# Kernel optimization log

Hardware: AMD Instinct MI355X
Metric: run time of the kernel (lower is better)

The kernel has to match this reference:

```python
import jax, jax.numpy as jnp
import numpy as np

D = 128
H = 4
DK = D // H


def _spmm(row, col, val, x, n):
    # sparse.mm(adj, x) with adj in COO form: out[row] += val * x[col]
    return jax.ops.segment_sum(val[:, None] * x[col], row, num_segments=n)


def _arrg(h, a1_w, a1_b, a2_w, a2_b):
    return jax.nn.leaky_relu(h @ a1_w + a1_b, negative_slope=0.01) @ a2_w + a2_b


def _cross_attn(x, q_x, q_w, k_w, v_w):
    n, d = x.shape
    m = q_x.shape[0]
    q = (q_x @ q_w).reshape(m, H, DK).transpose(1, 0, 2)   # [H, Q, dk]
    k = (x @ k_w).reshape(n, H, DK).transpose(1, 0, 2)     # [H, N, dk]
    v = (q_x @ v_w).reshape(m, H, DK).transpose(1, 0, 2)   # [H, Q, dk]
    s = jnp.einsum('hnd,hqd->hnq', k, q) / jnp.sqrt(jnp.float32(DK))
    w = jax.nn.softmax(s, axis=-1)                          # softmax over queries
    out = jnp.einsum('hnq,hqd->hnd', w, v).transpose(1, 0, 2).reshape(n, d)
    return out + x


def setup_inputs() -> dict:
    key = jax.random.key(0)
    ks = iter(jax.random.split(key, 64))
    nrm = lambda shape, s=0.05: jax.random.normal(next(ks), shape, jnp.float32) * s
    inp = {}
    inp['trans_w'] = nrm((1, D)); inp['trans_b'] = nrm((D,))
    inp['g_w'] = nrm((D, D));     inp['g_b'] = nrm((D,))
    inp['qg_w'] = nrm((D, D));    inp['qg_b'] = nrm((D,))
    inp['q_w'] = nrm((D, D)); inp['k_w'] = nrm((D, D)); inp['v_w'] = nrm((D, D))
    inp['a1_w'] = nrm((D, 2 * D)); inp['a1_b'] = nrm((2 * D,))
    inp['a2_w'] = nrm((2 * D, D)); inp['a2_b'] = nrm((D,))
    inp['x0'] = jax.random.normal(next(ks), (25000,), jnp.float32)
    inp['q0'] = jax.random.normal(next(ks), (100,), jnp.float32)
    for i in (1, 2, 3):
        inp[f'xin{i}'] = jax.random.normal(next(ks), (25000,), jnp.float32)
        inp[f'qin{i}'] = jax.random.normal(next(ks), (100,), jnp.float32)
    n_sizes = {1: 50000, 2: 75000, 3: 100000}
    q_sizes = {1: 200, 2: 300, 3: 400}
    for i in (1, 2, 3):
        e = 16 * n_sizes[i]
        inp[f'aval{i}'] = jax.random.uniform(next(ks), (e,), jnp.float32)
        inp[f'arow{i}'] = jax.random.randint(next(ks), (e,), 0, n_sizes[i], jnp.int64)
        inp[f'acol{i}'] = jax.random.randint(next(ks), (e,), 0, n_sizes[i], jnp.int64)
        qe = 16 * q_sizes[i]
        inp[f'qval{i}'] = jax.random.uniform(next(ks), (qe,), jnp.float32)
        inp[f'qrow{i}'] = jax.random.randint(next(ks), (qe,), 0, q_sizes[i], jnp.int64)
        inp[f'qcol{i}'] = jax.random.randint(next(ks), (qe,), 0, q_sizes[i], jnp.int64)
    return inp


def reference(trans_w, trans_b, g_w, g_b, qg_w, qg_b, q_w, k_w, v_w,
              a1_w, a1_b, a2_w, a2_b,
              x0, q0, xin1, xin2, xin3, qin1, qin2, qin3,
              aval1, aval2, aval3, qval1, qval2, qval3,
              arow1, acol1, arow2, acol2, arow3, acol3,
              qrow1, qcol1, qrow2, qcol2, qrow3, qcol3):
    trans = lambda v: v[:, None] @ trans_w + trans_b
    x = trans(x0)
    qx = trans(q0)
    steps = [
        (xin1, qin1, arow1, acol1, aval1, qrow1, qcol1, qval1, 50000, 200),
        (xin2, qin2, arow2, acol2, aval2, qrow2, qcol2, qval2, 75000, 300),
        (xin3, qin3, arow3, acol3, aval3, qrow3, qcol3, qval3, 100000, 400),
    ]
    for xin, qin, ar, ac, av, qr, qc, qv, n, m in steps:
        x = jnp.concatenate([x, trans(xin)], axis=0)
        qx = jnp.concatenate([qx, trans(qin)], axis=0)
        x = _spmm(ar, ac, av, x @ g_w + g_b, n)
        qx = _spmm(qr, qc, qv, qx @ qg_w + qg_b, m)
        x = _arrg(x, a1_w, a1_b, a2_w, a2_b)
        qx = _arrg(qx, a1_w, a1_b, a2_w, a2_b)
        x = _cross_attn(x, qx, q_w, k_w, v_w)
    return (x, qx)
```

## Files before the change

### kernel.cpp

```cpp
#include <hip/hip_runtime.h>

typedef unsigned short u16;
typedef __attribute__((ext_vector_type(8))) short bf16x8;
typedef __attribute__((ext_vector_type(4))) float f32x4;
typedef __attribute__((ext_vector_type(2))) unsigned u32x2;

__device__ __forceinline__ float b2f(u16 v) {
    return __uint_as_float(((unsigned)v) << 16);
}
__device__ __forceinline__ u16 f2b(float x) {
    unsigned u = __float_as_uint(x);
    unsigned r = u + 0x7FFFu + ((u >> 16) & 1u);
    return (u16)(r >> 16);
}
__device__ __forceinline__ float4 load_bf4(const u16* p) {
    ushort4 q = *(const ushort4*)p;
    float4 f;
    f.x = b2f(q.x); f.y = b2f(q.y); f.z = b2f(q.z); f.w = b2f(q.w);
    return f;
}
__device__ __forceinline__ float4 in4(const void* p, long off, bool bf) {
    if (bf) return load_bf4((const u16*)p + off);
    return *(const float4*)((const float*)p + off);
}
__device__ __forceinline__ float in1(const void* p, long off, bool bf) {
    if (bf) return b2f(((const u16*)p)[off]);
    return ((const float*)p)[off];
}
__device__ __forceinline__ int inIdx(const void* p, long i, bool i64) {
    return ((const int*)p)[i64 ? 2 * i : i];
}

__global__ void sniff_kernel(const u16* __restrict__ x0bits, const int* __restrict__ arow,
                             int* __restrict__ flags) {
    if (threadIdx.x != 0 || blockIdx.x != 0) return;
    int plaus = 0;
    for (int i = 0; i < 256; ++i) {
        u16 v = x0bits[i];
        int e = (v >> 7) & 0xFF;
        if (v == 0 || (e >= 100 && e <= 135)) plaus++;
    }
    flags[0] = (plaus >= 200) ? 1 : 0;
    int nz = 0;
    for (int i = 1; i < 128; i += 2) nz += (arow[i] != 0);
    flags[1] = (nz == 0) ? 1 : 0;
}

__global__ void trans_kernel(const void* __restrict__ v, const void* __restrict__ tw,
                             const void* __restrict__ tb, float* __restrict__ out,
                             int rows, const int* __restrict__ flags) {
    const bool bf = flags[0] != 0;
    int t = blockIdx.x * blockDim.x + threadIdx.x;
    int c4 = (t & 31) * 4;
    int r = t >> 5;
    if (r >= rows) return;
    float vv = in1(v, r, bf);
    float4 w4 = in4(tw, c4, bf);
    float4 b4 = in4(tb, c4, bf);
    float4 o;
    o.x = vv * w4.x + b4.x; o.y = vv * w4.y + b4.y;
    o.z = vv * w4.z + b4.z; o.w = vv * w4.w + b4.w;
    *(float4*)(out + (size_t)r * 128 + c4) = o;
}

__global__ void wprep_kernel(const void* __restrict__ src, u16* __restrict__ dst,
                             int K, int N, const int* __restrict__ flags) {
    const bool bf = flags[0] != 0;
    int idx = blockIdx.x * blockDim.x + threadIdx.x;
    if (idx >= K * N) return;
    int j = idx & 7, lane = (idx >> 3) & 63, t = idx >> 9;
    int KC = K >> 5;
    int kc = t % KC, ct = t / KC;
    int k = kc * 32 + (lane >> 4) * 8 + j;
    int nn = ct * 16 + (lane & 15);
    dst[idx] = f2b(in1(src, (long)k * N + nn, bf));
}

template<int KTOT, int NOUT, bool LEAKY, typename AT, typename CT>
__launch_bounds__(256)
__global__ void gemm_mfma_kernel(const AT* __restrict__ A, const u16* __restrict__ Wf,
                                 const void* __restrict__ bias, CT* __restrict__ C,
                                 int n, const int* __restrict__ flags) {
    constexpr int KC = KTOT / 32;
    constexpr int NT = NOUT / 16;
    __shared__ u16 wlds[KTOT * NOUT];
    {
        const int4* srcw = (const int4*)Wf;
        int4* dstw = (int4*)wlds;
        constexpr int NV = KTOT * NOUT * 2 / 16;
#pragma unroll
        for (int i = 0; i < NV / 256; ++i)
            dstw[i * 256 + threadIdx.x] = srcw[i * 256 + threadIdx.x];
    }
    __syncthreads();
    const bool bf = flags[0] != 0;
    const int lane = threadIdx.x & 63;
    const int wave = threadIdx.x >> 6;
    const int quad = lane >> 4, col = lane & 15;
    const int rbase = (blockIdx.x * 4 + wave) * 16;
    if (rbase >= n) return;
    int node = rbase + col; if (node >= n) node = n - 1;
    f32x4 acc[NT];
#pragma unroll
    for (int ct = 0; ct < NT; ++ct) acc[ct] = (f32x4){0.f, 0.f, 0.f, 0.f};
#pragma unroll
    for (int kc = 0; kc < KC; ++kc) {
        bf16x8 af;
        if constexpr (sizeof(AT) == 2) {
            af = *(const bf16x8*)((const u16*)A + (size_t)node * KTOT + kc * 32 + quad * 8);
        } else {
            const float* ap = (const float*)A + (size_t)node * KTOT + kc * 32 + quad * 8;
            float4 a0 = *(const float4*)ap;
            float4 a1 = *(const float4*)(ap + 4);
            af[0] = (short)f2b(a0.x); af[1] = (short)f2b(a0.y);
            af[2] = (short)f2b(a0.z); af[3] = (short)f2b(a0.w);
            af[4] = (short)f2b(a1.x); af[5] = (short)f2b(a1.y);
            af[6] = (short)f2b(a1.z); af[7] = (short)f2b(a1.w);
        }
#pragma unroll
        for (int ct = 0; ct < NT; ++ct) {
            bf16x8 wf = *(const bf16x8*)(wlds + (((ct * KC + kc) * 64 + lane) * 8));
            acc[ct] = __builtin_amdgcn_mfma_f32_16x16x32_bf16(af, wf, acc[ct], 0, 0, 0);
        }
    }
#pragma unroll
    for (int ct = 0; ct < NT; ++ct) {
        int colg = ct * 16 + col;
        float b = bias ? in1(bias, colg, bf) : 0.f;
#pragma unroll
        for (int r = 0; r < 4; ++r) {
            int row = rbase + quad * 4 + r;
            if (row >= n) continue;
            float v = acc[ct][r] + b;
            if (LEAKY) v = v > 0.f ? v : 0.01f * v;
            if constexpr (sizeof(CT) == 2) C[(size_t)row * NOUT + colg] = (CT)f2b(v);
            else                           C[(size_t)row * NOUT + colg] = (CT)v;
        }
    }
}

__launch_bounds__(256)
__global__ void gemm_qv_kernel(const float* __restrict__ A, const u16* __restrict__ Wfq,
                               const u16* __restrict__ Wfv, float* __restrict__ Cq,
                               float* __restrict__ Cv, int n) {
    __shared__ u16 wldsq[128 * 128];
    __shared__ u16 wldsv[128 * 128];
    {
        const int4* sq = (const int4*)Wfq;
        const int4* sv = (const int4*)Wfv;
        int4* dq = (int4*)wldsq;
        int4* dv = (int4*)wldsv;
#pragma unroll
        for (int i = 0; i < 8; ++i) {
            dq[i * 256 + threadIdx.x] = sq[i * 256 + threadIdx.x];
            dv[i * 256 + threadIdx.x] = sv[i * 256 + threadIdx.x];
        }
    }
    __syncthreads();
    const int lane = threadIdx.x & 63;
    const int wave = threadIdx.x >> 6;
    const int quad = lane >> 4, col = lane & 15;
    const int rbase = (blockIdx.x * 4 + wave) * 16;
    if (rbase >= n) return;
    int node = rbase + col; if (node >= n) node = n - 1;
    f32x4 accq[8], accv[8];
#pragma unroll
    for (int ct = 0; ct < 8; ++ct) {
        accq[ct] = (f32x4){0.f, 0.f, 0.f, 0.f};
        accv[ct] = (f32x4){0.f, 0.f, 0.f, 0.f};
    }
#pragma unroll
    for (int kc = 0; kc < 4; ++kc) {
        const float* ap = A + (size_t)node * 128 + kc * 32 + quad * 8;
        float4 a0 = *(const float4*)ap;
        float4 a1 = *(const float4*)(ap + 4);
        bf16x8 af;
        af[0] = (short)f2b(a0.x); af[1] = (short)f2b(a0.y);
        af[2] = (short)f2b(a0.z); af[3] = (short)f2b(a0.w);
        af[4] = (short)f2b(a1.x); af[5] = (short)f2b(a1.y);
        af[6] = (short)f2b(a1.z); af[7] = (short)f2b(a1.w);
#pragma unroll
        for (int ct = 0; ct < 8; ++ct) {
            bf16x8 wq = *(const bf16x8*)(wldsq + (((ct * 4 + kc) * 64 + lane) * 8));
            bf16x8 wv = *(const bf16x8*)(wldsv + (((ct * 4 + kc) * 64 + lane) * 8));
            accq[ct] = __builtin_amdgcn_mfma_f32_16x16x32_bf16(af, wq, accq[ct], 0, 0, 0);
            accv[ct] = __builtin_amdgcn_mfma_f32_16x16x32_bf16(af, wv, accv[ct], 0, 0, 0);
        }
    }
#pragma unroll
    for (int ct = 0; ct < 8; ++ct) {
        int colg = ct * 16 + col;
#pragma unroll
        for (int r = 0; r < 4; ++r) {
            int row = rbase + quad * 4 + r;
            if (row >= n) continue;
            Cq[(size_t)row * 128 + colg] = accq[ct][r];
            Cv[(size_t)row * 128 + colg] = accv[ct][r];
        }
    }
}

#define RSH 8
#define NBC_MAX 512
#define EPB 4096

__global__ void zero_int_kernel(int* __restrict__ p, int n) {
    int i = blockIdx.x * blockDim.x + threadIdx.x;
    if (i < n) p[i] = 0;
}

__global__ void bhist_kernel(const void* __restrict__ rows, int e, int* __restrict__ bcnt,
                             int nbc, const int* __restrict__ flags) {
    __shared__ int hist[NBC_MAX];
    const bool i64 = flags[1] != 0;
    for (int i = threadIdx.x; i < nbc; i += 256) hist[i] = 0;
    __syncthreads();
    int base = blockIdx.x * 8192;
    int end = base + 8192; if (end > e) end = e;
    for (int i = base + threadIdx.x; i < end; i += 256)
        atomicAdd(&hist[inIdx(rows, i, i64) >> RSH], 1);
    __syncthreads();
    for (int i = threadIdx.x; i < nbc; i += 256) {
        int c = hist[i];
        if (c) atomicAdd(&bcnt[i], c);
    }
}

__global__ void scanF_kernel(const int* __restrict__ bcnt, int nbc,
                             int* __restrict__ optr, int* __restrict__ ocur) {
    __shared__ int sc[NBC_MAX];
    const int tid = threadIdx.x;
    int v0 = (tid < nbc) ? bcnt[tid] : 0;
    int v1 = (tid + 256 < nbc) ? bcnt[tid + 256] : 0;
    sc[tid] = v0; sc[tid + 256] = v1;
    __syncthreads();
    for (int off = 1; off < NBC_MAX; off <<= 1) {
        int a = (tid >= off) ? sc[tid - off] : 0;
        int b = sc[tid + 256 - off];
        __syncthreads();
        sc[tid] += a;
        sc[tid + 256] += b;
        __syncthreads();
    }
    if (tid < nbc)       { int x = sc[tid] - v0;       optr[tid] = x;       ocur[tid] = x; }
    if (tid + 256 < nbc) { int x = sc[tid + 256] - v1; optr[tid + 256] = x; ocur[tid + 256] = x; }
}

__launch_bounds__(256)
__global__ void psort_kernel(const void* __restrict__ rows, const void* __restrict__ colsin,
                             const void* __restrict__ valsin, int e,
                             int* __restrict__ gcur, int2* __restrict__ pack0,
                             int nbc, const int* __restrict__ flags) {
    __shared__ int hist[NBC_MAX];
    __shared__ int scan[NBC_MAX];
    __shared__ int base[NBC_MAX];
    __shared__ int cur[NBC_MAX];
    __shared__ int2 stage[EPB];
    __shared__ u16 binof[EPB];
    const bool bf = flags[0] != 0;
    const bool i64 = flags[1] != 0;
    const int tid = threadIdx.x;
    const long s0 = (long)blockIdx.x * EPB;
    int cnt_e = e - (int)s0; if (cnt_e > EPB) cnt_e = EPB;

    for (int i = tid; i < NBC_MAX; i += 256) hist[i] = 0;
    __syncthreads();
    for (int j = tid; j < cnt_e; j += 256)
        atomicAdd(&hist[inIdx(rows, s0 + j, i64) >> RSH], 1);
    __syncthreads();
    for (int i = tid; i < NBC_MAX; i += 256) scan[i] = hist[i];
    __syncthreads();
    for (int off = 1; off < NBC_MAX; off <<= 1) {
        int a = (tid >= off) ? scan[tid - off] : 0;
        int c = scan[tid + 256 - off];
        __syncthreads();
        scan[tid] += a;
        scan[tid + 256] += c;
        __syncthreads();
    }
    for (int i = tid; i < nbc; i += 256) {
        int h = hist[i];
        cur[i] = scan[i] - h;
        base[i] = h ? atomicAdd(&gcur[i], h) : 0;
    }
    __syncthreads();
    for (int j = tid; j < cnt_e; j += 256) {
        int r = inIdx(rows, s0 + j, i64);
        int bin = r >> RSH;
        int p = atomicAdd(&cur[bin], 1);
        int2 pk;
        pk.x = ((r & ((1 << RSH) - 1)) << 20) | inIdx(colsin, s0 + j, i64);
        pk.y = __float_as_int(in1(valsin, s0 + j, bf));
        stage[p] = pk;
        binof[p] = (u16)bin;
    }
    __syncthreads();
    for (int j = tid; j < cnt_e; j += 256) {
        int bin = binof[j];
        int st = scan[bin] - hist[bin];
        pack0[base[bin] + (j - st)] = stage[j];
    }
}

__launch_bounds__(256)
__global__ void breorder256_kernel(const int2* __restrict__ pack0, const int* __restrict__ bptr,
                                   const int* __restrict__ bend, int2* __restrict__ pack1,
                                   int* __restrict__ rowptr, int* __restrict__ rowend, int n) {
    __shared__ int hist[256], scan[256], cur[256];
    const int b = blockIdx.x;
    const int s = bptr[b], e = bend[b];
    const int tid = threadIdx.x;
    hist[tid] = 0;
    __syncthreads();
    for (int i = s + tid; i < e; i += 256)
        atomicAdd(&hist[(unsigned)pack0[i].x >> 20], 1);
    __syncthreads();
    scan[tid] = hist[tid];
    __syncthreads();
    for (int off = 1; off < 256; off <<= 1) {
        int a = (tid >= off) ? scan[tid - off] : 0;
        __syncthreads();
        scan[tid] += a;
        __syncthreads();
    }
    int st = s + scan[tid] - hist[tid];
    cur[tid] = st;
    int rg = (b << RSH) + tid;
    if (rg < n) { rowptr[rg] = st; rowend[rg] = st + hist[tid]; }
    __syncthreads();
    for (int i = s + tid; i < e; i += 256) {
        int2 pk = pack0[i];
        int rl = (unsigned)pk.x >> 20;
        int p = atomicAdd(&cur[rl], 1);
        pack1[p] = (int2){pk.x & 0xFFFFF, pk.y};
    }
}

__device__ __forceinline__ f32x4 bffma4(float v, uint2 h, f32x4 a) {
    a[0] += v * __uint_as_float(h.x << 16);
    a[1] += v * __uint_as_float(h.x & 0xFFFF0000u);
    a[2] += v * __uint_as_float(h.y << 16);
    a[3] += v * __uint_as_float(h.y & 0xFFFF0000u);
    return a;
}
__global__ void spmm_kernel(const u16* __restrict__ H, const int* __restrict__ rowptr,
                            const int* __restrict__ rowend, const int2* __restrict__ pack,
                            u16* __restrict__ out, int n) {
    int w = threadIdx.x >> 6;
    int lane = threadIdx.x & 63;
    int r = blockIdx.x * 4 + w;
    if (r >= n) return;
    const int half = lane >> 5;
    const int l5 = lane & 31;
    int s = rowptr[r], e = rowend[r];
    f32x4 acc = {0.f, 0.f, 0.f, 0.f};
    int i = s + half;
    for (; i + 6 < e; i += 8) {
        int2 p0 = pack[i], p1 = pack[i + 2], p2 = pack[i + 4], p3 = pack[i + 6];
        uint2 h0 = *(const uint2*)(H + (size_t)p0.x * 128 + l5 * 4);
        uint2 h1 = *(const uint2*)(H + (size_t)p1.x * 128 + l5 * 4);
        uint2 h2 = *(const uint2*)(H + (size_t)p2.x * 128 + l5 * 4);
        uint2 h3 = *(const uint2*)(H + (size_t)p3.x * 128 + l5 * 4);
        acc = bffma4(__int_as_float(p0.y), h0, acc);
        acc = bffma4(__int_as_float(p1.y), h1, acc);
        acc = bffma4(__int_as_float(p2.y), h2, acc);
        acc = bffma4(__int_as_float(p3.y), h3, acc);
    }
    for (; i < e; i += 2) {
        int2 p0 = pack[i];
        uint2 h0 = *(const uint2*)(H + (size_t)p0.x * 128 + l5 * 4);
        acc = bffma4(__int_as_float(p0.y), h0, acc);
    }
    acc[0] += __shfl_xor(acc[0], 32, 64);
    acc[1] += __shfl_xor(acc[1], 32, 64);
    acc[2] += __shfl_xor(acc[2], 32, 64);
    acc[3] += __shfl_xor(acc[3], 32, 64);
    if (half == 0) {
        ushort4 o;
        o.x = f2b(acc[0]); o.y = f2b(acc[1]); o.z = f2b(acc[2]); o.w = f2b(acc[3]);
        *(ushort4*)(out + (size_t)r * 128 + l5 * 4) = o;
    }
}

__global__ void attn_prep_kernel(const float* __restrict__ Qq, const float* __restrict__ Qv,
                                 u16* __restrict__ Qf, u16* __restrict__ Vf,
                                 int m, int mt32) {
    int idx = blockIdx.x * blockDim.x + threadIdx.x;
    int total = 4 * mt32 * 1024;
    if (idx >= total) return;
    const int mt16 = mt32 * 2;
    const float scale = 0.17677669529663687f * 1.44269504088896340736f;
    {
        int j = idx & 7, lane = (idx >> 3) & 63;
        int t = idx >> 9;
        int h = t / mt16, qt = t - h * mt16;
        int dim = ((lane >> 4) & 3) * 8 + j;
        int query = qt * 16 + (lane & 15);
        Qf[idx] = (query < m) ? f2b(Qq[(size_t)query * 128 + h * 32 + dim] * scale) : (u16)0;
    }
    {
        int j = idx & 7, lane = (idx >> 3) & 63;
        int u = idx >> 9;
        int dh = u & 1, t = u >> 1;
        int h = t / mt32, qc = t - h * mt32;
        int query = qc * 32 + ((lane >> 4) & 3) * 8 + j;
        int dim = dh * 16 + (lane & 15);
        Vf[idx] = (query < m) ? f2b(Qv[(size_t)query * 128 + h * 32 + dim]) : (u16)0;
    }
}

__launch_bounds__(256)
__global__ void attn_mfma_kernel(const u16* __restrict__ Kb, const u16* __restrict__ Qf,
                                 const u16* __restrict__ Vf, float* __restrict__ X,
                                 int n, int m, int mt32, int pad) {
    __shared__ __align__(128) u16 Pbuf_all[4 * 1024];
    const int h = blockIdx.y;
    const int wave = threadIdx.x >> 6;
    const int lane = threadIdx.x & 63;
    const int nb = (blockIdx.x * 4 + wave) * 32;
    if (nb >= n) return;
    const int quad = lane >> 4, col = lane & 15;
    int node0 = nb + col;      if (node0 >= n) node0 = n - 1;
    int node1 = nb + 16 + col; if (node1 >= n) node1 = n - 1;
    bf16x8 kf0 = *(const bf16x8*)(Kb + (size_t)node0 * 128 + h * 32 + quad * 8);
    bf16x8 kf1 = *(const bf16x8*)(Kb + (size_t)node1 * 128 + h * 32 + quad * 8);
    f32x4 O00 = {0.f, 0.f, 0.f, 0.f}, O01 = {0.f, 0.f, 0.f, 0.f};
    f32x4 O10 = {0.f, 0.f, 0.f, 0.f}, O11 = {0.f, 0.f, 0.f, 0.f};
    const f32x4 zero = {0.f, 0.f, 0.f, 0.f};
    float Lp0[4] = {0.f, 0.f, 0.f, 0.f};
    float Lp1[4] = {0.f, 0.f, 0.f, 0.f};
    u16* Pw0 = Pbuf_all + wave * 1024;
    u16* Pw1 = Pw0 + 512;
    uint2* pw0[2]; uint2* pw1[2];
    pw0[0] = (uint2*)(Pw0 + col * 16 + quad * 4);
    pw0[1] = (uint2*)(Pw0 + 256 + col * 16 + quad * 4);
    pw1[0] = (uint2*)(Pw1 + col * 16 + quad * 4);
    pw1[1] = (uint2*)(Pw1 + 256 + col * 16 + quad * 4);
    const unsigned paddr0 = (unsigned)(uintptr_t)Pw0 + (unsigned)(quad * 256 + col * 8);
    const unsigned paddr1 = (unsigned)(uintptr_t)Pw1 + (unsigned)(quad * 256 + col * 8);
    const u16* Qbase = Qf + (size_t)h * (mt32 * 2) * 512;
    const u16* Vbase = Vf + (size_t)h * mt32 * 1024;
    for (int qc = 0; qc < mt32; ++qc) {
#pragma unroll
        for (int half = 0; half < 2; ++half) {
            bf16x8 qfr = *(const bf16x8*)(Qbase + (size_t)(qc * 2 + half) * 512 + lane * 8);
            f32x4 S0 = __builtin_amdgcn_mfma_f32_16x16x32_bf16(kf0, qfr, zero, 0, 0, 0);
            f32x4 S1 = __builtin_amdgcn_mfma_f32_16x16x32_bf16(kf1, qfr, zero, 0, 0, 0);
            float a0 = __builtin_amdgcn_exp2f(fminf(S0[0], 115.f));
            float a1 = __builtin_amdgcn_exp2f(fminf(S0[1], 115.f));
            float a2 = __builtin_amdgcn_exp2f(fminf(S0[2], 115.f));
            float a3 = __builtin_amdgcn_exp2f(fminf(S0[3], 115.f));
            float b0 = __builtin_amdgcn_exp2f(fminf(S1[0], 115.f));
            float b1 = __builtin_amdgcn_exp2f(fminf(S1[1], 115.f));
            float b2 = __builtin_amdgcn_exp2f(fminf(S1[2], 115.f));
            float b3 = __builtin_amdgcn_exp2f(fminf(S1[3], 115.f));
            Lp0[0] += a0; Lp0[1] += a1; Lp0[2] += a2; Lp0[3] += a3;
            Lp1[0] += b0; Lp1[1] += b1; Lp1[2] += b2; Lp1[3] += b3;
            unsigned ra, rb, rc, rd;
            asm volatile("v_cvt_pk_bf16_f32 %0, %1, %2" : "=v"(ra) : "v"(a0), "v"(a1));
            asm volatile("v_cvt_pk_bf16_f32 %0, %1, %2" : "=v"(rb) : "v"(a2), "v"(a3));
            asm volatile("v_cvt_pk_bf16_f32 %0, %1, %2" : "=v"(rc) : "v"(b0), "v"(b1));
            asm volatile("v_cvt_pk_bf16_f32 %0, %1, %2" : "=v"(rd) : "v"(b2), "v"(b3));
            uint2 pka; pka.x = ra; pka.y = rb;
            uint2 pkb; pkb.x = rc; pkb.y = rd;
            *pw0[half] = pka;
            *pw1[half] = pkb;
        }
        asm volatile("s_waitcnt lgkmcnt(0)" ::: "memory");
        u32x2 t0a, t0b, t1a, t1b;
        asm volatile("ds_read_b64_tr_b16 %0, %1" : "=&v"(t0a) : "v"(paddr0) : "memory");
        asm volatile("ds_read_b64_tr_b16 %0, %1 offset:128" : "=&v"(t0b) : "v"(paddr0) : "memory");
        asm volatile("ds_read_b64_tr_b16 %0, %1" : "=&v"(t1a) : "v"(paddr1) : "memory");
        asm volatile("ds_read_b64_tr_b16 %0, %1 offset:128" : "=&v"(t1b) : "v"(paddr1) : "memory");
        asm volatile("s_waitcnt lgkmcnt(0)" ::: "memory");
        __builtin_amdgcn_sched_barrier(0);
        bf16x8 pf0, pf1;
        ((u32x2*)&pf0)[0] = t0a; ((u32x2*)&pf0)[1] = t0b;
        ((u32x2*)&pf1)[0] = t1a; ((u32x2*)&pf1)[1] = t1b;
        bf16x8 v0 = *(const bf16x8*)(Vbase + (size_t)(qc * 2 + 0) * 512 + lane * 8);
        bf16x8 v1 = *(const bf16x8*)(Vbase + (size_t)(qc * 2 + 1) * 512 + lane * 8);
        O00 = __builtin_amdgcn_mfma_f32_16x16x32_bf16(pf0, v0, O00, 0, 0, 0);
        O01 = __builtin_amdgcn_mfma_f32_16x16x32_bf16(pf0, v1, O01, 0, 0, 0);
        O10 = __builtin_amdgcn_mfma_f32_16x16x32_bf16(pf1, v0, O10, 0, 0, 0);
        O11 = __builtin_amdgcn_mfma_f32_16x16x32_bf16(pf1, v1, O11, 0, 0, 0);
    }
#pragma unroll
    for (int mask = 1; mask < 16; mask <<= 1) {
#pragma unroll
        for (int r = 0; r < 4; ++r) {
            Lp0[r] += __shfl_xor(Lp0[r], mask, 64);
            Lp1[r] += __shfl_xor(Lp1[r], mask, 64);
        }
    }
#pragma unroll
    for (int r = 0; r < 4; ++r) {
        int nd = nb + quad * 4 + r;
        if (nd < n) {
            float inv = 1.f / fmaxf(Lp0[r] - (float)pad, 1e-35f);
            float* xp = X + (size_t)nd * 128 + h * 32;
            xp[col]      += O00[r] * inv;
            xp[16 + col] += O01[r] * inv;
        }
        int nd1 = nb + 16 + quad * 4 + r;
        if (nd1 < n) {
            float inv = 1.f / fmaxf(Lp1[r] - (float)pad, 1e-35f);
            float* xp = X + (size_t)nd1 * 128 + h * 32;
            xp[col]      += O10[r] * inv;
            xp[16 + col] += O11[r] * inv;
        }
    }
}

__global__ void out_writer_kernel(const float* __restrict__ in, void* __restrict__ out,
                                  long elem_off, int n4, const int* __restrict__ flags) {
    const bool bf = flags[0] != 0;
    int i = blockIdx.x * blockDim.x + threadIdx.x;
    if (i >= n4) return;
    float4 v = ((const float4*)in)[i];
    if (bf) {
        ushort4 q; q.x = f2b(v.x); q.y = f2b(v.y); q.z = f2b(v.z); q.w = f2b(v.w);
        ((ushort4*)((u16*)out + elem_off))[i] = q;
    } else {
        ((float4*)((float*)out + elem_off))[i] = v;
    }
}

extern "C" void kernel_launch(void* const* d_in, const int* in_sizes, int n_in,
                              void* d_out, int out_size, void* d_ws, size_t ws_size,
                              hipStream_t stream) {
    (void)n_in; (void)out_size; (void)ws_size;
    const void* trans_w = d_in[0];
    const void* trans_b = d_in[1];
    const void* g_w  = d_in[2];
    const void* g_b  = d_in[3];
    const void* qg_w = d_in[4];
    const void* qg_b = d_in[5];
    const void* q_w  = d_in[6];
    const void* k_w  = d_in[7];
    const void* v_w  = d_in[8];
    const void* a1_w = d_in[9];
    const void* a1_b = d_in[10];
    const void* a2_w = d_in[11];
    const void* a2_b = d_in[12];
    const void* x0   = d_in[13];
    const void* q0   = d_in[14];

    int ixin[3], iqin[3], iaval[3], iarow[3], iacol[3], iqval[3], iqrow[3], iqcol[3];
    if (in_sizes[16] == 100) {
        for (int s = 0; s < 3; ++s) {
            ixin[s] = 15 + 2 * s; iqin[s] = 16 + 2 * s;
            int b = 21 + 6 * s;
            iaval[s] = b; iarow[s] = b + 1; iacol[s] = b + 2;
            iqval[s] = b + 3; iqrow[s] = b + 4; iqcol[s] = b + 5;
        }
    } else {
        int xs[3] = {15,16,17}, qs_[3] = {18,19,20};
        int av[3] = {21,22,23}, qv[3] = {24,25,26};
        int ar[3] = {27,29,31}, ac[3] = {28,30,32};
        int qr[3] = {33,35,37}, qc[3] = {34,36,38};
        for (int s = 0; s < 3; ++s) {
            ixin[s]=xs[s]; iqin[s]=qs_[s]; iaval[s]=av[s]; iqval[s]=qv[s];
            iarow[s]=ar[s]; iacol[s]=ac[s]; iqrow[s]=qr[s]; iqcol[s]=qc[s];
        }
    }

    char* p = (char*)d_ws;
    auto alloc = [&](size_t bytes) -> char* {
        char* r = p;
        p += (bytes + 255) & ~(size_t)255;
        return r;
    };
    int*   flags = (int*)alloc(256);
    const int NMAX = 100000;
    float* X   = (float*)alloc((size_t)NMAX * 128 * 4);
    u16*   T1b = (u16*)  alloc((size_t)NMAX * 128 * 2);
    u16*   Xs  = (u16*)  alloc((size_t)NMAX * 128 * 2);
    u16*   T2  = (u16*)  alloc((size_t)NMAX * 256 * 2);
    float* QX  = (float*)alloc((size_t)400 * 128 * 4);
    u16*   QT1b= (u16*)  alloc((size_t)400 * 128 * 2);
    u16*   QXs = (u16*)  alloc((size_t)400 * 128 * 2);
    u16*   QT2 = (u16*)  alloc((size_t)400 * 256 * 2);
    float* Qq  = (float*)alloc((size_t)400 * 128 * 4);
    float* Qv  = (float*)alloc((size_t)400 * 128 * 4);
    u16*   Qfrag = (u16*)alloc((size_t)4 * 13 * 1024 * 2);
    u16*   Vfrag = (u16*)alloc((size_t)4 * 13 * 1024 * 2);
    u16* Wg  = (u16*)alloc((size_t)128 * 128 * 2);
    u16* Wqg = (u16*)alloc((size_t)128 * 128 * 2);
    u16* Wa1 = (u16*)alloc((size_t)128 * 256 * 2);
    u16* Wa2 = (u16*)alloc((size_t)256 * 128 * 2);
    u16* Wk  = (u16*)alloc((size_t)128 * 128 * 2);
    u16* Wq  = (u16*)alloc((size_t)128 * 128 * 2);
    u16* Wv  = (u16*)alloc((size_t)128 * 128 * 2);
    int2*  csr_pack = (int2*)alloc((size_t)1600000 * 8);
    int*   bcnt   = (int*)alloc((size_t)NBC_MAX * 4);
    int*   bktptr = (int*)alloc((size_t)NBC_MAX * 4);
    int*   bktcur = (int*)alloc((size_t)NBC_MAX * 4);
    int*   rowptr = (int*)alloc((size_t)NMAX * 4);
    int*   rowend = (int*)alloc((size_t)NMAX * 4);
    int2*  pack0  = (int2*)T2;

    sniff_kernel<<<1, 64, 0, stream>>>((const u16*)x0, (const int*)d_in[iarow[0]], flags);

    auto wprep = [&](const void* src, u16* dst, int K, int N) {
        wprep_kernel<<<(K * N + 255) / 256, 256, 0, stream>>>(src, dst, K, N, flags);
    };
    wprep(g_w,  Wg,  128, 128);
    wprep(qg_w, Wqg, 128, 128);
    wprep(a1_w, Wa1, 128, 256);
    wprep(a2_w, Wa2, 256, 128);
    wprep(k_w,  Wk,  128, 128);
    wprep(q_w,  Wq,  128, 128);
    wprep(v_w,  Wv,  128, 128);

    auto launch_trans = [&](const void* v, float* out, int rows) {
        trans_kernel<<<(rows * 32 + 255) / 256, 256, 0, stream>>>(v, trans_w, trans_b, out, rows, flags);
    };
    auto build_spmm = [&](const void* rows, const void* colsidx, const void* vals, int e,
                          int nrows, const u16* H, u16* OUT) {
        int nbc = (nrows + 255) >> RSH;
        zero_int_kernel<<<(nbc + 255) / 256, 256, 0, stream>>>(bcnt, nbc);
        bhist_kernel<<<(e + 8191) / 8192, 256, 0, stream>>>(rows, e, bcnt, nbc, flags);
        scanF_kernel<<<1, 256, 0, stream>>>(bcnt, nbc, bktptr, bktcur);
        psort_kernel<<<(e + EPB - 1) / EPB, 256, 0, stream>>>(rows, colsidx, vals, e,
                                                              bktcur, pack0, nbc, flags);
        breorder256_kernel<<<nbc, 256, 0, stream>>>(pack0, bktptr, bktcur, csr_pack,
                                                    rowptr, rowend, nrows);
        spmm_kernel<<<(nrows + 3) / 4, 256, 0, stream>>>(H, rowptr, rowend, csr_pack,
                                                         OUT, nrows);
    };

    int nprev = in_sizes[13];
    int mprev = in_sizes[14];
    launch_trans(x0, X, nprev);
    launch_trans(q0, QX, mprev);

    const int ns[3] = {50000, 75000, 100000};
    const int ms[3] = {200, 300, 400};
    for (int s = 0; s < 3; ++s) {
        const int n = ns[s], m = ms[s];
        const int e  = in_sizes[iaval[s]];
        const int qe = in_sizes[iqval[s]];
        launch_trans(d_in[ixin[s]], X + (size_t)nprev * 128, n - nprev);
        launch_trans(d_in[iqin[s]], QX + (size_t)mprev * 128, m - mprev);
        const int gb  = (n + 63) / 64;
        const int gqb = (m + 63) / 64;
        gemm_mfma_kernel<128, 128, false, float, u16><<<gb, 256, 0, stream>>>(X, Wg, g_b, T1b, n, flags);
        build_spmm(d_in[iarow[s]], d_in[iacol[s]], d_in[iaval[s]], e, n, T1b, Xs);
        gemm_mfma_kernel<128, 128, false, float, u16><<<gqb, 256, 0, stream>>>(QX, Wqg, qg_b, QT1b, m, flags);
        build_spmm(d_in[iqrow[s]], d_in[iqcol[s]], d_in[iqval[s]], qe, m, QT1b, QXs);
        gemm_mfma_kernel<128, 256, true, u16, u16><<<gb, 256, 0, stream>>>(Xs, Wa1, a1_b, T2, n, flags);
        gemm_mfma_kernel<256, 128, false, u16, float><<<gb, 256, 0, stream>>>(T2, Wa2, a2_b, X, n, flags);
        gemm_mfma_kernel<128, 256, true, u16, u16><<<gqb, 256, 0, stream>>>(QXs, Wa1, a1_b, QT2, m, flags);
        gemm_mfma_kernel<256, 128, false, u16, float><<<gqb, 256, 0, stream>>>(QT2, Wa2, a2_b, QX, m, flags);
        gemm_mfma_kernel<128, 128, false, float, u16><<<gb, 256, 0, stream>>>(X, Wk, nullptr, T1b, n, flags);
        gemm_qv_kernel<<<gqb, 256, 0, stream>>>(QX, Wq, Wv, Qq, Qv, m);
        const int mt32 = (m + 31) / 32;
        const int pad = mt32 * 32 - m;
        const int ptot = 4 * mt32 * 1024;
        attn_prep_kernel<<<(ptot + 255) / 256, 256, 0, stream>>>(Qq, Qv, Qfrag, Vfrag, m, mt32);
        attn_mfma_kernel<<<dim3((n + 127) / 128, 4), 256, 0, stream>>>(T1b, Qfrag, Vfrag, X, n, m, mt32, pad);
        nprev = n;
        mprev = m;
    }

    const int n4x = 100000 * 128 / 4;
    const int n4q = 400 * 128 / 4;
    out_writer_kernel<<<(n4x + 255) / 256, 256, 0, stream>>>(X, d_out, 0, n4x, flags);
    out_writer_kernel<<<(n4q + 255) / 256, 256, 0, stream>>>(QX, d_out, (long)100000 * 128, n4q, flags);
}
```

Baseline: 1.282 ms.

## Build small query CSR in one kernel and widen spmm gathers to 16B

For the small query graphs (at most 512 rows), the five-kernel bucket sort is replaced by one single-block kernel. It builds a row histogram in shared memory, scans it, and scatters the column/value pairs into CSR order, which cuts several launches per step. The spmm kernel now splits each wavefront into four groups of 16 lanes. Each lane gathers 8 bf16 values with a 16-byte load, which halves the number of load instructions per row. The price is more accumulator registers and an extra shuffle level in the final reduction.

```diff
diff --git a/kernel.cpp b/kernel.cpp
--- a/kernel.cpp
+++ b/kernel.cpp
@@ -244,6 +244,47 @@
     }
     if (tid < nbc)       { int x = sc[tid] - v0;       optr[tid] = x;       ocur[tid] = x; }
     if (tid + 256 < nbc) { int x = sc[tid + 256] - v1; optr[tid + 256] = x; ocur[tid + 256] = x; }
+}
+
+__launch_bounds__(256)
+__global__ void qbuild_kernel(const void* __restrict__ rows, const void* __restrict__ colsin,
+                              const void* __restrict__ valsin, int e, int nrows,
+                              int2* __restrict__ pack1, int* __restrict__ rowptr,
+                              int* __restrict__ rowend, const int* __restrict__ flags) {
+    __shared__ int hist[512], cur[512], sc[512];
+    const bool bf = flags[0] != 0;
+    const bool i64 = flags[1] != 0;
+    const int tid = threadIdx.x;
+    for (int i = tid; i < 512; i += 256) hist[i] = 0;
+    __syncthreads();
+    for (int i = tid; i < e; i += 256)
+        atomicAdd(&hist[inIdx(rows, i, i64)], 1);
+    __syncthreads();
+    int v0 = hist[tid], v1 = hist[tid + 256];
+    sc[tid] = v0; sc[tid + 256] = v1;
+    __syncthreads();
+    for (int off = 1; off < 512; off <<= 1) {
+        int a = (tid >= off) ? sc[tid - off] : 0;
+        int b = sc[tid + 256 - off];
+        __syncthreads();
+        sc[tid] += a;
+        sc[tid + 256] += b;
+        __syncthreads();
+    }
+    {
+        int x = sc[tid] - v0;
+        cur[tid] = x;
+        if (tid < nrows) { rowptr[tid] = x; rowend[tid] = x + v0; }
+        int x1 = sc[tid + 256] - v1;
+        cur[tid + 256] = x1;
+        if (tid + 256 < nrows) { rowptr[tid + 256] = x1; rowend[tid + 256] = x1 + v1; }
+    }
+    __syncthreads();
+    for (int i = tid; i < e; i += 256) {
+        int r = inIdx(rows, i, i64);
+        int p = atomicAdd(&cur[r], 1);
+        pack1[p] = (int2){inIdx(colsin, i, i64), __float_as_int(in1(valsin, i, bf))};
+    }
 }
 
 __launch_bounds__(256)
@@ -336,12 +377,15 @@
     }
 }
 
-__device__ __forceinline__ f32x4 bffma4(float v, uint2 h, f32x4 a) {
+__device__ __forceinline__ void bffma8(float v, uint4 h, float* a) {
     a[0] += v * __uint_as_float(h.x << 16);
     a[1] += v * __uint_as_float(h.x & 0xFFFF0000u);
     a[2] += v * __uint_as_float(h.y << 16);
     a[3] += v * __uint_as_float(h.y & 0xFFFF0000u);
-    return a;
+    a[4] += v * __uint_as_float(h.z << 16);
+    a[5] += v * __uint_as_float(h.z & 0xFFFF0000u);
+    a[6] += v * __uint_as_float(h.w << 16);
+    a[7] += v * __uint_as_float(h.w & 0xFFFF0000u);
 }
 __global__ void spmm_kernel(const u16* __restrict__ H, const int* __restrict__ rowptr,
                             const int* __restrict__ rowend, const int2* __restrict__ pack,
@@ -350,35 +394,39 @@
     int lane = threadIdx.x & 63;
     int r = blockIdx.x * 4 + w;
     if (r >= n) return;
-    const int half = lane >> 5;
-    const int l5 = lane & 31;
+    const int s16 = lane >> 4;
+    const int l16 = lane & 15;
     int s = rowptr[r], e = rowend[r];
-    f32x4 acc = {0.f, 0.f, 0.f, 0.f};
-    int i = s + half;
-    for (; i + 6 < e; i += 8) {
-        int2 p0 = pack[i], p1 = pack[i + 2], p2 = pack[i + 4], p3 = pack[i + 6];
-        uint2 h0 = *(const uint2*)(H + (size_t)p0.x * 128 + l5 * 4);
-        uint2 h1 = *(const uint2*)(H + (size_t)p1.x * 128 + l5 * 4);
-        uint2 h2 = *(const uint2*)(H + (size_t)p2.x * 128 + l5 * 4);
-        uint2 h3 = *(const uint2*)(H + (size_t)p3.x * 128 + l5 * 4);
-        acc = bffma4(__int_as_float(p0.y), h0, acc);
-        acc = bffma4(__int_as_float(p1.y), h1, acc);
-        acc = bffma4(__int_as_float(p2.y), h2, acc);
-        acc = bffma4(__int_as_float(p3.y), h3, acc);
-    }
-    for (; i < e; i += 2) {
+    float a[8] = {0.f, 0.f, 0.f, 0.f, 0.f, 0.f, 0.f, 0.f};
+    int i = s + s16;
+    for (; i + 12 < e; i += 16) {
+        int2 p0 = pack[i], p1 = pack[i + 4], p2 = pack[i + 8], p3 = pack[i + 12];
+        uint4 h0 = *(const uint4*)(H + (size_t)p0.x * 128 + l16 * 8);
+        uint4 h1 = *(const uint4*)(H + (size_t)p1.x * 128 + l16 * 8);
+        uint4 h2 = *(const uint4*)(H + (size_t)p2.x * 128 + l16 * 8);
+        uint4 h3 = *(const uint4*)(H + (size_t)p3.x * 128 + l16 * 8);
+        bffma8(__int_as_float(p0.y), h0, a);
+        bffma8(__int_as_float(p1.y), h1, a);
+        bffma8(__int_as_float(p2.y), h2, a);
+        bffma8(__int_as_float(p3.y), h3, a);
+    }
+    for (; i < e; i += 4) {
         int2 p0 = pack[i];
-        uint2 h0 = *(const uint2*)(H + (size_t)p0.x * 128 + l5 * 4);
-        acc = bffma4(__int_as_float(p0.y), h0, acc);
-    }
-    acc[0] += __shfl_xor(acc[0], 32, 64);
-    acc[1] += __shfl_xor(acc[1], 32, 64);
-    acc[2] += __shfl_xor(acc[2], 32, 64);
-    acc[3] += __shfl_xor(acc[3], 32, 64);
-    if (half == 0) {
-        ushort4 o;
-        o.x = f2b(acc[0]); o.y = f2b(acc[1]); o.z = f2b(acc[2]); o.w = f2b(acc[3]);
-        *(ushort4*)(out + (size_t)r * 128 + l5 * 4) = o;
+        uint4 h0 = *(const uint4*)(H + (size_t)p0.x * 128 + l16 * 8);
+        bffma8(__int_as_float(p0.y), h0, a);
+    }
+#pragma unroll
+    for (int k = 0; k < 8; ++k) {
+        a[k] += __shfl_xor(a[k], 16, 64);
+        a[k] += __shfl_xor(a[k], 32, 64);
+    }
+    if (s16 == 0) {
+        uint4 o;
+        o.x = (unsigned)f2b(a[0]) | ((unsigned)f2b(a[1]) << 16);
+        o.y = (unsigned)f2b(a[2]) | ((unsigned)f2b(a[3]) << 16);
+        o.z = (unsigned)f2b(a[4]) | ((unsigned)f2b(a[5]) << 16);
+        o.w = (unsigned)f2b(a[6]) | ((unsigned)f2b(a[7]) << 16);
+        *(uint4*)(out + (size_t)r * 128 + l16 * 8) = o;
     }
 }
 
@@ -617,14 +665,19 @@
     };
     auto build_spmm = [&](const void* rows, const void* colsidx, const void* vals, int e,
                           int nrows, const u16* H, u16* OUT) {
-        int nbc = (nrows + 255) >> RSH;
-        zero_int_kernel<<<(nbc + 255) / 256, 256, 0, stream>>>(bcnt, nbc);
-        bhist_kernel<<<(e + 8191) / 8192, 256, 0, stream>>>(rows, e, bcnt, nbc, flags);
-        scanF_kernel<<<1, 256, 0, stream>>>(bcnt, nbc, bktptr, bktcur);
-        psort_kernel<<<(e + EPB - 1) / EPB, 256, 0, stream>>>(rows, colsidx, vals, e,
-                                                              bktcur, pack0, nbc, flags);
-        breorder256_kernel<<<nbc, 256, 0, stream>>>(pack0, bktptr, bktcur, csr_pack,
-                                                    rowptr, rowend, nrows);
+        if (nrows <= 512) {
+            qbuild_kernel<<<1, 256, 0, stream>>>(rows, colsidx, vals, e, nrows,
+                                                 csr_pack, rowptr, rowend, flags);
+        } else {
+            int nbc = (nrows + 255) >> RSH;
+            zero_int_kernel<<<(nbc + 255) / 256, 256, 0, stream>>>(bcnt, nbc);
+            bhist_kernel<<<(e + 8191) / 8192, 256, 0, stream>>>(rows, e, bcnt, nbc, flags);
+            scanF_kernel<<<1, 256, 0, stream>>>(bcnt, nbc, bktptr, bktcur);
+            psort_kernel<<<(e + EPB - 1) / EPB, 256, 0, stream>>>(rows, colsidx, vals, e,
+                                                                  bktcur, pack0, nbc, flags);
+            breorder256_kernel<<<nbc, 256, 0, stream>>>(pack0, bktptr, bktcur, csr_pack,
+                                                        rowptr, rowend, nrows);
+        }
         spmm_kernel<<<(nrows + 3) / 4, 256, 0, stream>>>(H, rowptr, rowend, csr_pack,
                                                          OUT, nrows);
     };
```

Measured after the change: 1.218 ms. 5.0% less time.
